# Kernel optimization log

Measured on AMD Instinct MI355X. Metric: run time of the kernel, lower is better.

Reference implementation:

```python
import jax, jax.numpy as jnp
import numpy as np

DIM = 2048        # config.dim
HID = 1408        # config.moe_inter_dim
E = 16            # config.n_routed_experts
TOPK = 4          # config.n_activated_experts
SHARED = 2816     # n_shared_experts * moe_inter_dim
B, S = 1, 2048
ROUTE_SCALE = 1.0


def setup_inputs() -> dict:
    key = jax.random.key(0)
    ks = jax.random.split(key, 8)
    def w(k, shape, fan_in):
        return jax.random.normal(k, shape, jnp.float32) * (1.0 / np.sqrt(fan_in))
    return {
        "x": jax.random.normal(ks[0], (B, S, DIM), jnp.float32),
        "gate_w": w(ks[1], (E, DIM), DIM),
        "w1": w(ks[2], (E, HID, DIM), DIM),   # per-expert nn.Linear(dim, hid).weight
        "w2": w(ks[3], (E, DIM, HID), HID),   # per-expert nn.Linear(hid, dim).weight
        "w3": w(ks[4], (E, HID, DIM), DIM),
        "sw1": w(ks[5], (SHARED, DIM), DIM),  # shared MLP weights
        "sw2": w(ks[6], (DIM, SHARED), SHARED),
        "sw3": w(ks[7], (SHARED, DIM), DIM),
    }


def reference(x, gate_w, w1, w2, w3, sw1, sw2, sw3):
    shape = x.shape
    xt = x.reshape(-1, DIM)                      # [T, D]
    T = xt.shape[0]

    # --- Gate (score_func='softmax', n_groups=1, bias=None since dim != 7168) ---
    logits = xt @ gate_w.T                        # [T, E]
    scores = jax.nn.softmax(logits.astype(jnp.float32), axis=-1)
    topv, idx = jax.lax.top_k(scores, TOPK)       # n_groups==1: topk over flat scores
    weights = topv * ROUTE_SCALE                  # gather(original_scores, idx) == topv here

    # aux load-balance loss
    tpe = jnp.zeros((E,), jnp.float32).at[idx.reshape(-1)].add(1.0) / (T * TOPK)
    aux_loss = E * jnp.sum(tpe * scores.mean(axis=0))

    # --- Routed experts: combine weights [T, E], then batched SwiGLU GEMMs ---
    comb = jnp.zeros((T, E), jnp.float32).at[jnp.arange(T)[:, None], idx].add(weights)
    h = jax.nn.silu(jnp.einsum('td,ehd->teh', xt, w1)) * jnp.einsum('td,ehd->teh', xt, w3)
    y = jnp.einsum('teh,edh,te->td', h, w2, comb)  # weighted combine (0-weight experts cancel)

    # --- Shared experts (SwiGLU MLP, dropout=0) ---
    z = (jax.nn.silu(xt @ sw1.T) * (xt @ sw3.T)) @ sw2.T

    return (y + z).reshape(shape), aux_loss
```

## Files before the change

kernel.cpp:

```cpp
#include <hip/hip_runtime.h>
#include <hip/hip_bf16.h>

typedef unsigned short u16;
typedef __attribute__((ext_vector_type(8))) short short8;
typedef __attribute__((ext_vector_type(4))) float f32x4;

#define DIM 2048
#define HID 1408
#define NE 16
#define NTOK 2048
#define TOPK_ 4
#define SHID 2816
#define CAPROWS 10240
#define MAXTILES (CAPROWS / 128)
#define AUX_IDX (2048 * 2048)

__device__ inline u16 f2bf(float f) {
  __bf16 h = (__bf16)f;
  return __builtin_bit_cast(u16, h);
}

__device__ inline void gload_lds16(const void* g, void* l) {
  __builtin_amdgcn_global_load_lds(
      (const __attribute__((address_space(1))) unsigned int*)g,
      (__attribute__((address_space(3))) unsigned int*)l, 16, 0, 0);
}

__device__ inline void cvt8_store(const float* __restrict__ in, u16* __restrict__ out, long i) {
  float4 a = *(const float4*)(in + i);
  float4 b = *(const float4*)(in + i + 4);
  union { u16 u[8]; uint4 v; } o;
  o.u[0] = f2bf(a.x); o.u[1] = f2bf(a.y); o.u[2] = f2bf(a.z); o.u[3] = f2bf(a.w);
  o.u[4] = f2bf(b.x); o.u[5] = f2bf(b.y); o.u[6] = f2bf(b.z); o.u[7] = f2bf(b.w);
  *(uint4*)(out + i) = o.v;
}

__global__ __launch_bounds__(256) void gatecvt_kernel(
    const float* __restrict__ x, const float* __restrict__ gw,
    double* __restrict__ logits, u16* __restrict__ xb) {
  if ((int)blockIdx.x >= NTOK) {
    long i0 = ((long)(blockIdx.x - NTOK) * 256 + threadIdx.x) * 8;
    long stride = (long)(gridDim.x - NTOK) * 2048;
    for (long i = i0; i < (long)NTOK * DIM; i += stride) cvt8_store(x, xb, i);
    return;
  }
  int t = blockIdx.x;
  const float* xt = x + (size_t)t * DIM;
  __shared__ double red[NE][4];
  int lane = threadIdx.x & 63, wid = threadIdx.x >> 6;
  for (int e = 0; e < NE; ++e) {
    const float* w = gw + e * DIM;
    double p = 0.0;
    for (int d = threadIdx.x; d < DIM; d += 256)
      p += (double)xt[d] * (double)w[d];
#pragma unroll
    for (int s = 32; s; s >>= 1) p += __shfl_xor(p, s);
    if (lane == 0) red[e][wid] = p;
  }
  __syncthreads();
  if (threadIdx.x < NE)
    logits[(size_t)t * NE + threadIdx.x] =
        red[threadIdx.x][0] + red[threadIdx.x][1] + red[threadIdx.x][2] + red[threadIdx.x][3];
}

__global__ __launch_bounds__(256) void topk_kernel(
    const double* __restrict__ logits,
    int* __restrict__ idxb, float* __restrict__ wtb,
    int* __restrict__ counts, float* __restrict__ ssum) {
  __shared__ int lcnt[NE];
  __shared__ float lsum[NE];
  if (threadIdx.x < NE) { lcnt[threadIdx.x] = 0; lsum[threadIdx.x] = 0.f; }
  __syncthreads();
  int t = blockIdx.x * 256 + threadIdx.x;
  int lane = threadIdx.x & 63;
  double sc[NE];
  double m = -1e300;
#pragma unroll
  for (int e = 0; e < NE; ++e) {
    sc[e] = logits[(size_t)t * NE + e];
    if (sc[e] > m) m = sc[e];
  }
  double s = 0.0;
#pragma unroll
  for (int e = 0; e < NE; ++e) { sc[e] = exp(sc[e] - m); s += sc[e]; }
  double inv = 1.0 / s;
#pragma unroll
  for (int e = 0; e < NE; ++e) sc[e] *= inv;
  unsigned used = 0;
  for (int k = 0; k < TOPK_; ++k) {
    int be = 0; double bv = -1.0;
#pragma unroll
    for (int e = 0; e < NE; ++e)
      if (!((used >> e) & 1u) && sc[e] > bv) { bv = sc[e]; be = e; }
    used |= 1u << be;
    idxb[t * TOPK_ + k] = be;
    wtb[t * TOPK_ + k] = (float)bv;
    atomicAdd(&lcnt[be], 1);
  }
#pragma unroll
  for (int e = 0; e < NE; ++e) {
    float v = (float)sc[e];
#pragma unroll
    for (int sft = 32; sft; sft >>= 1) v += __shfl_xor(v, sft);
    if (lane == 0) atomicAdd(&lsum[e], v);
  }
  __syncthreads();
  if (threadIdx.x < NE) {
    atomicAdd(&counts[threadIdx.x], lcnt[threadIdx.x]);
    atomicAdd(&ssum[threadIdx.x], lsum[threadIdx.x]);
  }
}

__global__ __launch_bounds__(256) void setup_kernel(
    const int* __restrict__ counts, int* __restrict__ off, int* __restrict__ cap,
    const float* __restrict__ ssum, int* __restrict__ perm, float* __restrict__ pwt,
    float* __restrict__ aux_out,
    int* __restrict__ tile2e, int* __restrict__ tile2m0) {
  for (int i = threadIdx.x; i < MAXTILES; i += 256) tile2e[i] = -1;
  __syncthreads();
  if (threadIdx.x == 0) {
    int o = 0; double aux = 0.0; int nt = 0;
    for (int e = 0; e < NE; ++e) {
      off[e] = o;
      int c = (counts[e] + 127) & ~127;
      cap[e] = c;
      for (int t = 0; t < (c >> 7); ++t) {
        int slot = (nt / 10) + (nt % 10) * 8;
        tile2e[slot] = e;
        tile2m0[slot] = o + t * 128;
        ++nt;
      }
      o += c;
      aux += ((double)counts[e] / (NTOK * TOPK_)) * ((double)ssum[e] / NTOK);
    }
    aux_out[0] = (float)(NE * aux);
  }
  for (int i = threadIdx.x; i < CAPROWS; i += 256) { perm[i] = 0; pwt[i] = 0.f; }
}

__global__ __launch_bounds__(256) void scatter_kernel(
    const int* __restrict__ idxb, const float* __restrict__ wtb,
    const int* __restrict__ off, int* __restrict__ cursor,
    int* __restrict__ perm, float* __restrict__ pwt) {
  int t = blockIdx.x * 256 + threadIdx.x;
  if (t >= NTOK) return;
  for (int k = 0; k < TOPK_; ++k) {
    int e = idxb[t * TOPK_ + k];
    int s = atomicAdd(&cursor[e], 1);
    int p = off[e] + s;
    perm[p] = t;
    pwt[p] = wtb[t * TOPK_ + k];
  }
}

template <bool GATHER, bool DUAL, int EPI>
__global__ __launch_bounds__(512) void gemm12_kernel(
    const u16* __restrict__ A, int lda,
    const float* __restrict__ B1, const float* __restrict__ B3,
    int ldb, long bstride, int K,
    const int* __restrict__ tile2e, const int* __restrict__ tile2m0,
    const int* __restrict__ seg_off, const int* __restrict__ seg_cnt,
    const int* __restrict__ perm, const float* __restrict__ pwt,
    float* __restrict__ C0, int ldc0,
    u16* __restrict__ Cb, int ldcb, int Mfixed) {
  int e, m0, rowlim;
  if (tile2e) {
    e = tile2e[blockIdx.x];
    if (e < 0) return;
    m0 = tile2m0[blockIdx.x];
    rowlim = seg_off[e] + seg_cnt[e];
  } else {
    e = 0;
    m0 = blockIdx.x * 128;
    if (m0 >= Mfixed) return;
    rowlim = Mfixed;
  }
  int n0 = blockIdx.y * 64;
  const float* Bb1 = B1 + (long)e * bstride;
  const float* Bb3 = DUAL ? (B3 + (long)e * bstride) : nullptr;

  __shared__ u16 As[2][128 * 64];
  __shared__ u16 Bs1[64 * 64];
  __shared__ u16 Bs3[DUAL ? 64 * 64 : 1];

  int tid = threadIdx.x;
  int lane = tid & 63;
  int wid = tid >> 6;
  int wr = wid >> 1, wc = wid & 1;

  f32x4 acc1[2][2], acc3[2][2];
#pragma unroll
  for (int mi = 0; mi < 2; ++mi)
#pragma unroll
    for (int ni = 0; ni < 2; ++ni) {
      acc1[mi][ni] = (f32x4){0.f, 0.f, 0.f, 0.f};
      acc3[mi][ni] = (f32x4){0.f, 0.f, 0.f, 0.f};
    }

  int sr = tid >> 3;
  int scA = tid & 7;
  long abase[2];
#pragma unroll
  for (int it = 0; it < 2; ++it) {
    int row = m0 + it * 64 + sr;
    int rid = GATHER ? perm[row] : row;
    abase[it] = (long)rid * lda + ((scA ^ (sr & 7)) << 3);
  }
  int brr = tid >> 4;
  int gB = tid & 15;
  int wofs = (((gB >> 1) ^ (brr & 7)) << 3) + ((gB & 1) << 2);
  long bbase[2];
#pragma unroll
  for (int it = 0; it < 2; ++it)
    bbase[it] = (long)(n0 + it * 32 + brr) * ldb + gB * 4;

  float4 R1a[2], R3a[2], R1b[2], R3b[2];

  auto stageA = [&](int buf, int k0) {
#pragma unroll
    for (int it = 0; it < 2; ++it)
      gload_lds16(A + abase[it] + k0, &As[buf][(it * 64 + sr) * 64 + scA * 8]);
  };
  auto loadB = [&](float4 (&r1)[2], float4 (&r3)[2], int k0) {
#pragma unroll
    for (int it = 0; it < 2; ++it) r1[it] = *(const float4*)(Bb1 + bbase[it] + k0);
    if (DUAL) {
#pragma unroll
      for (int it = 0; it < 2; ++it) r3[it] = *(const float4*)(Bb3 + bbase[it] + k0);
    }
  };
  auto writeB = [&](float4 (&r1)[2], float4 (&r3)[2]) {
#pragma unroll
    for (int it = 0; it < 2; ++it) {
      int lo = (it * 32 + brr) * 64 + wofs;
      ushort4 o;
      o.x = f2bf(r1[it].x); o.y = f2bf(r1[it].y); o.z = f2bf(r1[it].z); o.w = f2bf(r1[it].w);
      *(ushort4*)&Bs1[lo] = o;
      if (DUAL) {
        ushort4 q;
        q.x = f2bf(r3[it].x); q.y = f2bf(r3[it].y); q.z = f2bf(r3[it].z); q.w = f2bf(r3[it].w);
        *(ushort4*)&Bs3[lo] = q;
      }
    }
  };
  auto compute = [&](int cur) {
#pragma unroll
    for (int kk = 0; kk < 64; kk += 32) {
      short8 af[2], b1f[2], b3f[2];
#pragma unroll
      for (int i = 0; i < 2; ++i) {
        int R = wr * 32 + i * 16 + (lane & 15);
        int c = (kk >> 3) + (lane >> 4);
        af[i] = *(const short8*)&As[cur][R * 64 + ((c ^ (R & 7)) << 3)];
      }
#pragma unroll
      for (int i = 0; i < 2; ++i) {
        int r = wc * 32 + i * 16 + (lane & 15);
        int cR = (kk >> 3) + (lane >> 4);
        b1f[i] = *(const short8*)&Bs1[r * 64 + ((cR ^ (r & 7)) << 3)];
        if (DUAL)
          b3f[i] = *(const short8*)&Bs3[r * 64 + ((cR ^ (r & 7)) << 3)];
      }
#pragma unroll
      for (int mi = 0; mi < 2; ++mi)
#pragma unroll
        for (int ni = 0; ni < 2; ++ni) {
          acc1[mi][ni] = __builtin_amdgcn_mfma_f32_16x16x32_bf16(af[mi], b1f[ni], acc1[mi][ni], 0, 0, 0);
          if (DUAL)
            acc3[mi][ni] = __builtin_amdgcn_mfma_f32_16x16x32_bf16(af[mi], b3f[ni], acc3[mi][ni], 0, 0, 0);
        }
    }
  };

  int NT = K >> 6;
  loadB(R1a, R3a, 0);
  stageA(0, 0);
  loadB(R1b, R3b, 64);

#define GEMM12_STEP(T, CUR, RB1, RB3)                                         \
  {                                                                           \
    int t_ = (T);                                                             \
    writeB(RB1, RB3);                           \
    bool hasA = (t_ + 1 < NT), hasB = (t_ + 2 < NT);                          \
    if (hasA) stageA((CUR) ^ 1, (t_ + 1) << 6);                               \
    if (hasB) loadB(RB1, RB3, (t_ + 2) << 6);                                 \
    if (hasB) {                                                               \
      if (DUAL) asm volatile("s_waitcnt vmcnt(10)" ::: "memory");             \
      else      asm volatile("s_waitcnt vmcnt(6)" ::: "memory");              \
    } else if (hasA) {                                                        \
      if (DUAL) asm volatile("s_waitcnt vmcnt(6)" ::: "memory");              \
      else      asm volatile("s_waitcnt vmcnt(4)" ::: "memory");              \
    } else {                                                                  \
      asm volatile("s_waitcnt vmcnt(0)" ::: "memory");                        \
    }                                                                         \
    asm volatile("s_waitcnt lgkmcnt(0)" ::: "memory");                        \
    __builtin_amdgcn_sched_barrier(0);                                        \
    __builtin_amdgcn_s_barrier();                    \
    __builtin_amdgcn_sched_barrier(0);                                        \
    compute(CUR);                                                             \
    __builtin_amdgcn_sched_barrier(0);                                        \
    __builtin_amdgcn_s_barrier();           \
  }

  for (int t = 0; t < NT; t += 2) {
    GEMM12_STEP(t,     0, R1a, R3a);
    GEMM12_STEP(t + 1, 1, R1b, R3b);
  }
#undef GEMM12_STEP

  int rbase = m0 + wr * 32 + (lane >> 4) * 4;
  int cbase = n0 + wc * 32 + (lane & 15);
#pragma unroll
  for (int mi = 0; mi < 2; ++mi) {
#pragma unroll
    for (int ni = 0; ni < 2; ++ni) {
      int col = cbase + ni * 16;
#pragma unroll
      for (int r = 0; r < 4; ++r) {
        int row = rbase + mi * 16 + r;
        float v = acc1[mi][ni][r];
        if (EPI == 0) {
          float a3 = acc3[mi][ni][r];
          float sg = v / (1.f + __expf(-v));
          Cb[(long)row * ldcb + col] = f2bf(sg * a3);
        } else if (EPI == 1) {
          C0[(long)row * ldc0 + col] = v;
        } else {
          if (row < rowlim) {
            atomicAdd(&C0[(long)perm[row] * ldc0 + col], v * pwt[row]);
          }
        }
      }
    }
  }
}

extern "C" void kernel_launch(void* const* d_in, const int* in_sizes, int n_in,
                              void* d_out, int out_size, void* d_ws, size_t ws_size,
                              hipStream_t stream) {
  (void)in_sizes; (void)n_in; (void)out_size; (void)ws_size;
  const float* x   = (const float*)d_in[0];
  const float* gw  = (const float*)d_in[1];
  const float* w1  = (const float*)d_in[2];
  const float* w2  = (const float*)d_in[3];
  const float* w3  = (const float*)d_in[4];
  const float* sw1 = (const float*)d_in[5];
  const float* sw2 = (const float*)d_in[6];
  const float* sw3 = (const float*)d_in[7];
  float* out = (float*)d_out;
  char* ws = (char*)d_ws;

  int*   counts = (int*)(ws + 0);
  int*   cursor = (int*)(ws + 64);
  int*   off    = (int*)(ws + 128);
  int*   cap    = (int*)(ws + 192);
  float* ssum   = (float*)(ws + 256);
  int*   tile2e = (int*)(ws + 1024);
  int*   tile2m0= (int*)(ws + 2048);
  int*   idxb   = (int*)(ws + 4096);
  float* wtb    = (float*)(ws + 4096 + 32768);
  int*   perm   = (int*)(ws + 4096 + 65536);
  float* pwt    = (float*)(ws + 4096 + 65536 + 40960);
  u16*   xb     = (u16*)(ws + 262144);
  double* logits = (double*)(ws + 8650752);
  u16*   hbuf   = (u16*)(ws + 16777216);
  u16*   hsb    = (u16*)(ws + 45613056);

  hipMemsetAsync(ws, 0, 512, stream);
  gatecvt_kernel<<<dim3(NTOK + 128), dim3(256), 0, stream>>>(x, gw, logits, xb);
  topk_kernel<<<dim3(NTOK / 256), dim3(256), 0, stream>>>(logits, idxb, wtb, counts, ssum);
  setup_kernel<<<dim3(1), dim3(256), 0, stream>>>(counts, off, cap, ssum, perm, pwt,
                                                  out + AUX_IDX, tile2e, tile2m0);
  scatter_kernel<<<dim3(8), dim3(256), 0, stream>>>(idxb, wtb, off, cursor, perm, pwt);

  gemm12_kernel<true, true, 0><<<dim3(MAXTILES, HID / 64), dim3(512), 0, stream>>>(
      xb, DIM, w1, w3, DIM, (long)HID * DIM, DIM, tile2e, tile2m0,
      off, counts, perm, pwt, nullptr, 0, hbuf, HID, 0);
  gemm12_kernel<false, true, 0><<<dim3(NTOK / 128, SHID / 64), dim3(512), 0, stream>>>(
      xb, DIM, sw1, sw3, DIM, 0, DIM, nullptr, nullptr,
      nullptr, nullptr, nullptr, nullptr, nullptr, 0, hsb, SHID, NTOK);
  gemm12_kernel<false, false, 1><<<dim3(NTOK / 128, DIM / 64), dim3(512), 0, stream>>>(
      hsb, SHID, sw2, nullptr, SHID, 0, SHID, nullptr, nullptr,
      nullptr, nullptr, nullptr, nullptr, out, DIM, nullptr, 0, NTOK);
  gemm12_kernel<false, false, 2><<<dim3(MAXTILES, DIM / 64), dim3(512), 0, stream>>>(
      hbuf, HID, w2, nullptr, HID, (long)DIM * HID, HID, tile2e, tile2m0,
      off, counts, perm, pwt, out, DIM, nullptr, 0, 0);
}
```

Before: 576.7 us.

## Double GEMM workgroup to 16 waves with smaller per-wave tiles

Doubles threads per workgroup to 1024 so 16 waves each compute a 32x16 sub-tile of the same 128x64 block tile, halving per-thread staging loads and accumulators. The intent is more latency hiding and lower register pressure per wave. In exchange, A fragments are read from LDS by more waves, so there is more LDS traffic per MFMA, and barrier synchronization spans more waves.

```diff
diff --git a/kernel.cpp b/kernel.cpp
--- a/kernel.cpp
+++ b/kernel.cpp
@@ -154,7 +154,7 @@
 }
 
 template <bool GATHER, bool DUAL, int EPI>
-__global__ __launch_bounds__(512) void gemm12_kernel(
+__global__ __launch_bounds__(1024) void gemm13_kernel(
     const u16* __restrict__ A, int lda,
     const float* __restrict__ B1, const float* __restrict__ B3,
     int ldb, long bstride, int K,
@@ -186,89 +186,71 @@
   int tid = threadIdx.x;
   int lane = tid & 63;
   int wid = tid >> 6;
-  int wr = wid >> 1, wc = wid & 1;
-
-  f32x4 acc1[2][2], acc3[2][2];
-#pragma unroll
-  for (int mi = 0; mi < 2; ++mi)
-#pragma unroll
-    for (int ni = 0; ni < 2; ++ni) {
-      acc1[mi][ni] = (f32x4){0.f, 0.f, 0.f, 0.f};
-      acc3[mi][ni] = (f32x4){0.f, 0.f, 0.f, 0.f};
-    }
+  int wr = wid >> 2, wc = wid & 3;
+
+  f32x4 acc1[2], acc3[2];
+#pragma unroll
+  for (int mi = 0; mi < 2; ++mi) {
+    acc1[mi] = (f32x4){0.f, 0.f, 0.f, 0.f};
+    acc3[mi] = (f32x4){0.f, 0.f, 0.f, 0.f};
+  }
 
   int sr = tid >> 3;
   int scA = tid & 7;
-  long abase[2];
-#pragma unroll
-  for (int it = 0; it < 2; ++it) {
-    int row = m0 + it * 64 + sr;
+  long abase;
+  {
+    int row = m0 + sr;
     int rid = GATHER ? perm[row] : row;
-    abase[it] = (long)rid * lda + ((scA ^ (sr & 7)) << 3);
+    abase = (long)rid * lda + ((scA ^ (sr & 7)) << 3);
   }
   int brr = tid >> 4;
   int gB = tid & 15;
   int wofs = (((gB >> 1) ^ (brr & 7)) << 3) + ((gB & 1) << 2);
-  long bbase[2];
-#pragma unroll
-  for (int it = 0; it < 2; ++it)
-    bbase[it] = (long)(n0 + it * 32 + brr) * ldb + gB * 4;
-
-  float4 R1a[2], R3a[2], R1b[2], R3b[2];
+  long bbase = (long)(n0 + brr) * ldb + gB * 4;
+
+  float4 R1a, R3a, R1b, R3b;
 
   auto stageA = [&](int buf, int k0) {
-#pragma unroll
-    for (int it = 0; it < 2; ++it)
-      gload_lds16(A + abase[it] + k0, &As[buf][(it * 64 + sr) * 64 + scA * 8]);
+    gload_lds16(A + abase + k0, &As[buf][sr * 64 + scA * 8]);
   };
-  auto loadB = [&](float4 (&r1)[2], float4 (&r3)[2], int k0) {
-#pragma unroll
-    for (int it = 0; it < 2; ++it) r1[it] = *(const float4*)(Bb1 + bbase[it] + k0);
+  auto loadB = [&](float4& r1, float4& r3, int k0) {
+    r1 = *(const float4*)(Bb1 + bbase + k0);
+    if (DUAL) r3 = *(const float4*)(Bb3 + bbase + k0);
+  };
+  auto writeB = [&](float4& r1, float4& r3) {
+    int lo = brr * 64 + wofs;
+    ushort4 o;
+    o.x = f2bf(r1.x); o.y = f2bf(r1.y); o.z = f2bf(r1.z); o.w = f2bf(r1.w);
+    *(ushort4*)&Bs1[lo] = o;
     if (DUAL) {
-#pragma unroll
-      for (int it = 0; it < 2; ++it) r3[it] = *(const float4*)(Bb3 + bbase[it] + k0);
-    }
-  };
-  auto writeB = [&](float4 (&r1)[2], float4 (&r3)[2]) {
-#pragma unroll
-    for (int it = 0; it < 2; ++it) {
-      int lo = (it * 32 + brr) * 64 + wofs;
-      ushort4 o;
-      o.x = f2bf(r1[it].x); o.y = f2bf(r1[it].y); o.z = f2bf(r1[it].z); o.w = f2bf(r1[it].w);
-      *(ushort4*)&Bs1[lo] = o;
-      if (DUAL) {
-        ushort4 q;
-        q.x = f2bf(r3[it].x); q.y = f2bf(r3[it].y); q.z = f2bf(r3[it].z); q.w = f2bf(r3[it].w);
-        *(ushort4*)&Bs3[lo] = q;
-      }
+      ushort4 q;
+      q.x = f2bf(r3.x); q.y = f2bf(r3.y); q.z = f2bf(r3.z); q.w = f2bf(r3.w);
+      *(ushort4*)&Bs3[lo] = q;
     }
   };
   auto compute = [&](int cur) {
 #pragma unroll
     for (int kk = 0; kk < 64; kk += 32) {
-      short8 af[2], b1f[2], b3f[2];
+      short8 af[2], b1f, b3f;
 #pragma unroll
       for (int i = 0; i < 2; ++i) {
         int R = wr * 32 + i * 16 + (lane & 15);
         int c = (kk >> 3) + (lane >> 4);
         af[i] = *(const short8*)&As[cur][R * 64 + ((c ^ (R & 7)) << 3)];
       }
-#pragma unroll
-      for (int i = 0; i < 2; ++i) {
-        int r = wc * 32 + i * 16 + (lane & 15);
+      {
+        int r = wc * 16 + (lane & 15);
         int cR = (kk >> 3) + (lane >> 4);
-        b1f[i] = *(const short8*)&Bs1[r * 64 + ((cR ^ (r & 7)) << 3)];
+        b1f = *(const short8*)&Bs1[r * 64 + ((cR ^ (r & 7)) << 3)];
         if (DUAL)
-          b3f[i] = *(const short8*)&Bs3[r * 64 + ((cR ^ (r & 7)) << 3)];
-      }
-#pragma unroll
-      for (int mi = 0; mi < 2; ++mi)
-#pragma unroll
-        for (int ni = 0; ni < 2; ++ni) {
-          acc1[mi][ni] = __builtin_amdgcn_mfma_f32_16x16x32_bf16(af[mi], b1f[ni], acc1[mi][ni], 0, 0, 0);
-          if (DUAL)
-            acc3[mi][ni] = __builtin_amdgcn_mfma_f32_16x16x32_bf16(af[mi], b3f[ni], acc3[mi][ni], 0, 0, 0);
-        }
+          b3f = *(const short8*)&Bs3[r * 64 + ((cR ^ (r & 7)) << 3)];
+      }
+#pragma unroll
+      for (int mi = 0; mi < 2; ++mi) {
+        acc1[mi] = __builtin_amdgcn_mfma_f32_16x16x32_bf16(af[mi], b1f, acc1[mi], 0, 0, 0);
+        if (DUAL)
+          acc3[mi] = __builtin_amdgcn_mfma_f32_16x16x32_bf16(af[mi], b3f, acc3[mi], 0, 0, 0);
+      }
     }
   };
 
@@ -277,7 +259,7 @@
   stageA(0, 0);
   loadB(R1b, R3b, 64);
 
-#define GEMM12_STEP(T, CUR, RB1, RB3)                                         \
+#define GEMM13_STEP(T, CUR, RB1, RB3)                                         \
   {                                                                           \
     int t_ = (T);                                                             \
     writeB(RB1, RB3);                           \
@@ -285,11 +267,11 @@
     if (hasA) stageA((CUR) ^ 1, (t_ + 1) << 6);                               \
     if (hasB) loadB(RB1, RB3, (t_ + 2) << 6);                                 \
     if (hasB) {                                                               \
-      if (DUAL) asm volatile("s_waitcnt vmcnt(10)" ::: "memory");             \
-      else      asm volatile("s_waitcnt vmcnt(6)" ::: "memory");              \
+      if (DUAL) asm volatile("s_waitcnt vmcnt(5)" ::: "memory");              \
+      else      asm volatile("s_waitcnt vmcnt(3)" ::: "memory");              \
     } else if (hasA) {                                                        \
-      if (DUAL) asm volatile("s_waitcnt vmcnt(6)" ::: "memory");              \
-      else      asm volatile("s_waitcnt vmcnt(4)" ::: "memory");              \
+      if (DUAL) asm volatile("s_waitcnt vmcnt(3)" ::: "memory");              \
+      else      asm volatile("s_waitcnt vmcnt(2)" ::: "memory");              \
     } else {                                                                  \
       asm volatile("s_waitcnt vmcnt(0)" ::: "memory");                        \
     }                                                                         \
@@ -303,32 +285,28 @@
   }
 
   for (int t = 0; t < NT; t += 2) {
-    GEMM12_STEP(t,     0, R1a, R3a);
-    GEMM12_STEP(t + 1, 1, R1b, R3b);
-  }
-#undef GEMM12_STEP
+    GEMM13_STEP(t,     0, R1a, R3a);
+    GEMM13_STEP(t + 1, 1, R1b, R3b);
+  }
+#undef GEMM13_STEP
 
   int rbase = m0 + wr * 32 + (lane >> 4) * 4;
-  int cbase = n0 + wc * 32 + (lane & 15);
+  int col = n0 + wc * 16 + (lane & 15);
 #pragma unroll
   for (int mi = 0; mi < 2; ++mi) {
 #pragma unroll
-    for (int ni = 0; ni < 2; ++ni) {
-      int col = cbase + ni * 16;
-#pragma unroll
-      for (int r = 0; r < 4; ++r) {
-        int row = rbase + mi * 16 + r;
-        float v = acc1[mi][ni][r];
-        if (EPI == 0) {
-          float a3 = acc3[mi][ni][r];
-          float sg = v / (1.f + __expf(-v));
-          Cb[(long)row * ldcb + col] = f2bf(sg * a3);
-        } else if (EPI == 1) {
-          C0[(long)row * ldc0 + col] = v;
-        } else {
-          if (row < rowlim) {
-            atomicAdd(&C0[(long)perm[row] * ldc0 + col], v * pwt[row]);
-          }
+    for (int r = 0; r < 4; ++r) {
+      int row = rbase + mi * 16 + r;
+      float v = acc1[mi][r];
+      if (EPI == 0) {
+        float a3 = acc3[mi][r];
+        float sg = v / (1.f + __expf(-v));
+        Cb[(long)row * ldcb + col] = f2bf(sg * a3);
+      } else if (EPI == 1) {
+        C0[(long)row * ldc0 + col] = v;
+      } else {
+        if (row < rowlim) {
+          atomicAdd(&C0[(long)perm[row] * ldc0 + col], v * pwt[row]);
         }
       }
     }
@@ -373,16 +351,16 @@
                                                   out + AUX_IDX, tile2e, tile2m0);
   scatter_kernel<<<dim3(8), dim3(256), 0, stream>>>(idxb, wtb, off, cursor, perm, pwt);
 
-  gemm12_kernel<true, true, 0><<<dim3(MAXTILES, HID / 64), dim3(512), 0, stream>>>(
+  gemm13_kernel<true, true, 0><<<dim3(MAXTILES, HID / 64), dim3(1024), 0, stream>>>(
       xb, DIM, w1, w3, DIM, (long)HID * DIM, DIM, tile2e, tile2m0,
       off, counts, perm, pwt, nullptr, 0, hbuf, HID, 0);
-  gemm12_kernel<false, true, 0><<<dim3(NTOK / 128, SHID / 64), dim3(512), 0, stream>>>(
+  gemm13_kernel<false, true, 0><<<dim3(NTOK / 128, SHID / 64), dim3(1024), 0, stream>>>(
       xb, DIM, sw1, sw3, DIM, 0, DIM, nullptr, nullptr,
       nullptr, nullptr, nullptr, nullptr, nullptr, 0, hsb, SHID, NTOK);
-  gemm12_kernel<false, false, 1><<<dim3(NTOK / 128, DIM / 64), dim3(512), 0, stream>>>(
+  gemm13_kernel<false, false, 1><<<dim3(NTOK / 128, DIM / 64), dim3(1024), 0, stream>>>(
       hsb, SHID, sw2, nullptr, SHID, 0, SHID, nullptr, nullptr,
       nullptr, nullptr, nullptr, nullptr, out, DIM, nullptr, 0, NTOK);
-  gemm12_kernel<false, false, 2><<<dim3(MAXTILES, DIM / 64), dim3(512), 0, stream>>>(
+  gemm13_kernel<false, false, 2><<<dim3(MAXTILES, DIM / 64), dim3(1024), 0, stream>>>(
       hbuf, HID, w2, nullptr, HID, (long)DIM * HID, HID, tile2e, tile2m0,
       off, counts, perm, pwt, out, DIM, nullptr, 0, 0);
 }
```

After: 658.7 us. 1.14x slower.
